# Kernel optimization log

Hardware: AMD Instinct MI355X
Metric: run time of the kernel (lower is better)

The kernel has to match this reference:

```python
import jax, jax.numpy as jnp
import numpy as np

B, T, C = 16, 2048, 384
E = 8          # num_experts
TOP_K = 2
CAP_F = 1.0
D_FF = 4 * C   # 1536


def setup_inputs() -> dict:
    key = jax.random.key(0)
    ks = jax.random.split(key, 10)
    s = 0.02
    return {
        "x": jax.random.normal(ks[0], (B, T, C), dtype=jnp.float32),
        "noise": jax.random.normal(ks[1], (B, T, E), dtype=jnp.float32),
        "w_route": jax.random.normal(ks[2], (C, E), dtype=jnp.float32) * s,
        "b_route": jnp.zeros((E,), dtype=jnp.float32),
        "w_noise": jax.random.normal(ks[3], (C, E), dtype=jnp.float32) * s,
        "b_noise": jnp.zeros((E,), dtype=jnp.float32),
        "w1": jax.random.normal(ks[4], (E, C, D_FF), dtype=jnp.float32) * s,
        "b1": jnp.zeros((E, D_FF), dtype=jnp.float32),
        "w2": jax.random.normal(ks[5], (E, D_FF, C), dtype=jnp.float32) * s,
        "b2": jnp.zeros((E, C), dtype=jnp.float32),
    }


def _moe_forward(x, noise, w_route, b_route, w_noise, b_noise, w1, b1, w2, b2):
    Bx, Tx, Cx = x.shape
    N = Bx * Tx
    cap = int(N * TOP_K / E * CAP_F)  # static expert capacity

    # --- NoisyTopkRouter ---
    logits = jnp.einsum('btc,ce->bte', x, w_route) + b_route
    noise_logits = jnp.einsum('btc,ce->bte', x, w_noise) + b_noise
    noisy = logits + noise * jax.nn.softplus(noise_logits)
    topv, topi = jax.lax.top_k(noisy, TOP_K)                    # [B,T,K]
    keep_mask = jnp.any(jax.nn.one_hot(topi, E, dtype=jnp.bool_), axis=-2)  # [B,T,E]
    sparse_logits = jnp.where(keep_mask, noisy, -jnp.inf)
    gating = jax.nn.softmax(sparse_logits, axis=-1)             # [B,T,E]

    # --- dispatch by top-1 expert with capacity drop (eval: dropout off) ---
    flat_x = x.reshape(N, Cx)
    flat_g = gating.reshape(N, E)
    top1 = jnp.argmax(flat_g, axis=-1)                          # [N]
    token_ids = jnp.arange(N, dtype=jnp.int32)
    out = jnp.zeros_like(flat_x)

    for i in range(E):
        mask = top1 == i                                        # [N]
        pos = jnp.cumsum(mask) - 1                              # rank within expert
        keep = mask & (pos < cap)
        slot = jnp.where(keep, pos, cap)                        # overflow -> dummy slot
        buf = jnp.zeros((cap + 1,), dtype=jnp.int32).at[slot].set(token_ids)
        idx = buf[:cap]                                         # token id per capacity slot
        valid = (jnp.arange(cap) < jnp.sum(keep))[:, None]      # [cap,1]
        xi = flat_x[idx]                                        # [cap,C] gather
        h = jnp.square(jax.nn.relu(xi @ w1[i] + b1[i]))         # ReLU^2
        yi = h @ w2[i] + b2[i]                                  # [cap,C]
        weighted = yi * flat_g[idx, i][:, None] * valid
        out = out.at[idx].add(weighted)                         # scatter-add

    return out.reshape(Bx, Tx, Cx)


def reference(x, noise, w_route, b_route, w_noise, b_noise, w1, b1, w2, b2):
    return _moe_forward(x, noise, w_route, b_route, w_noise, b_noise, w1, b1, w2, b2)
```

## Files before the change

kernel.cpp:

```cpp
#include <hip/hip_runtime.h>
#include <stdint.h>

#define E_NUM 8
#define CAP 8192
#define NTOK 32768
#define CDIM 384
#define DFF 1536
#define CNT_PAD 64

typedef unsigned short u16;
typedef __attribute__((ext_vector_type(8))) short short8;
typedef __attribute__((ext_vector_type(4))) float f32x4;

__device__ inline u16 f2bf(float f) {
    uint32_t u = __builtin_bit_cast(uint32_t, f);
    u += 0x7fffu + ((u >> 16) & 1u);
    return (u16)(u >> 16);
}

__device__ inline void gload_lds16(const void* g, void* l) {
    __builtin_amdgcn_global_load_lds(
        (const __attribute__((address_space(1))) void*)(uintptr_t)g,
        (__attribute__((address_space(3))) void*)(uint32_t)(uintptr_t)l,
        16, 0, 0);
}

__device__ inline void expert_span(const int* __restrict__ cnt, int e,
                                   int& base, int& n_e) {
    base = 0; n_e = 0;
#pragma unroll
    for (int i = 0; i < E_NUM; ++i) {
        int n = min(cnt[i * CNT_PAD], CAP);
        if (i < e) base += (n + 127) & ~127;
        else if (i == e) n_e = n;
    }
}

#define RT_TOK 64
#define RT_KC 64
#define RT_XS 68

__global__ __launch_bounds__(256, 3) void routing_kernel(
    const float* __restrict__ x, const float* __restrict__ noise,
    const float* __restrict__ w_route, const float* __restrict__ b_route,
    const float* __restrict__ w_noise, const float* __restrict__ b_noise,
    int* __restrict__ cnt, int* __restrict__ list, float* __restrict__ gate,
    u16* __restrict__ xbf)
{
    __shared__ float xs[RT_TOK * RT_XS];
    __shared__ float ws_r[CDIM * E_NUM];
    __shared__ float ws_n[CDIM * E_NUM];
    int tid = threadIdx.x;
    int lane = tid & 63;
    int seg = __builtin_amdgcn_readfirstlane(tid >> 6);
    int tok = tid & 63;
    int t0 = blockIdx.x * RT_TOK;

#pragma unroll
    for (int i = 0; i < 3; ++i) {
        int idx = tid + i * 256;
        *(float4*)&ws_r[idx * 4] = ((const float4*)w_route)[idx];
        *(float4*)&ws_n[idx * 4] = ((const float4*)w_noise)[idx];
    }

    int srow = tid >> 4;
    int scol = (tid & 15) * 4;

    float ar[E_NUM], an[E_NUM];
#pragma unroll
    for (int e = 0; e < E_NUM; ++e) { ar[e] = 0.f; an[e] = 0.f; }

    for (int c = 0; c < CDIM / RT_KC; ++c) {
        __syncthreads();
#pragma unroll
        for (int p = 0; p < 4; ++p) {
            int row = p * 16 + srow;
            float4 v = *(const float4*)(x + (size_t)(t0 + row) * CDIM + c * RT_KC + scol);
            *(float4*)&xs[row * RT_XS + scol] = v;
            uint2 b;
            b.x = (uint32_t)f2bf(v.x) | ((uint32_t)f2bf(v.y) << 16);
            b.y = (uint32_t)f2bf(v.z) | ((uint32_t)f2bf(v.w) << 16);
            *(uint2*)(xbf + (size_t)(t0 + row) * CDIM + c * RT_KC + scol) = b;
        }
        __syncthreads();
#pragma unroll
        for (int q = 0; q < 4; ++q) {
            float4 xq = *(const float4*)&xs[tok * RT_XS + seg * 16 + q * 4];
            int kb = c * RT_KC + seg * 16 + q * 4;
#pragma unroll
            for (int jj = 0; jj < 4; ++jj) {
                const float* wrk = &ws_r[(kb + jj) * E_NUM];
                const float* wnk = &ws_n[(kb + jj) * E_NUM];
                float4 wa = *(const float4*)wrk, wb = *(const float4*)(wrk + 4);
                float4 na = *(const float4*)wnk, nb = *(const float4*)(wnk + 4);
                float xk = (jj == 0) ? xq.x : (jj == 1) ? xq.y : (jj == 2) ? xq.z : xq.w;
                ar[0] += xk * wa.x; ar[1] += xk * wa.y; ar[2] += xk * wa.z; ar[3] += xk * wa.w;
                ar[4] += xk * wb.x; ar[5] += xk * wb.y; ar[6] += xk * wb.z; ar[7] += xk * wb.w;
                an[0] += xk * na.x; an[1] += xk * na.y; an[2] += xk * na.z; an[3] += xk * na.w;
                an[4] += xk * nb.x; an[5] += xk * nb.y; an[6] += xk * nb.z; an[7] += xk * nb.w;
            }
        }
    }
    __syncthreads();
    float* part = xs;
    float* pp = part + (size_t)(seg * 64 + tok) * 16;
    *(f32x4*)&pp[0]  = (f32x4){ar[0], ar[1], ar[2], ar[3]};
    *(f32x4*)&pp[4]  = (f32x4){ar[4], ar[5], ar[6], ar[7]};
    *(f32x4*)&pp[8]  = (f32x4){an[0], an[1], an[2], an[3]};
    *(f32x4*)&pp[12] = (f32x4){an[4], an[5], an[6], an[7]};
    __syncthreads();
    if (seg == 0) {
        int t = t0 + lane;
        float sr[E_NUM], sn[E_NUM];
#pragma unroll
        for (int e = 0; e < E_NUM; ++e) { sr[e] = b_route[e]; sn[e] = b_noise[e]; }
#pragma unroll
        for (int s = 0; s < 4; ++s) {
            const float* q = part + (size_t)(s * 64 + lane) * 16;
#pragma unroll
            for (int e = 0; e < E_NUM; ++e) { sr[e] += q[e]; sn[e] += q[8 + e]; }
        }
        float nz[E_NUM];
        const float* np = noise + (size_t)t * E_NUM;
#pragma unroll
        for (int e = 0; e < E_NUM; ++e) {
            float s = sn[e];
            float sp = fmaxf(s, 0.f) + __logf(1.f + __expf(-fabsf(s)));
            nz[e] = sr[e] + np[e] * sp;
        }
        float v1 = -1e30f; int i1 = 0;
#pragma unroll
        for (int e = 0; e < E_NUM; ++e) if (nz[e] > v1) { v1 = nz[e]; i1 = e; }
        float v2 = -1e30f;
#pragma unroll
        for (int e = 0; e < E_NUM; ++e) if (e != i1 && nz[e] > v2) v2 = nz[e];
        gate[t] = 1.f / (1.f + __expf(v2 - v1));
#pragma unroll
        for (int e = 0; e < E_NUM; ++e) {
            unsigned long long m = __ballot(i1 == e);
            if (m == 0) continue;
            int cnum = __popcll(m);
            int leader = __ffsll((long long)m) - 1;
            int basec = 0;
            if (lane == leader) basec = atomicAdd(&cnt[e * CNT_PAD], cnum);
            basec = __shfl(basec, leader);
            if (i1 == e) {
                int pos = basec + __popcll(m & ((1ull << lane) - 1ull));
                if (pos < CAP) list[e * CAP + pos] = t;
            }
        }
    }
}

__global__ __launch_bounds__(256) void transpose_cvt_kernel(
    const float* __restrict__ w1, u16* __restrict__ W1t,
    const float* __restrict__ w2, u16* __restrict__ W2t)
{
    __shared__ float tile[32][33];
    int z = blockIdx.z;
    const float* in; u16* out; int R, S, r0, c0;
    if (z < E_NUM) {
        in = w1 + (size_t)z * CDIM * DFF;  out = W1t + (size_t)z * CDIM * DFF;
        R = CDIM; S = DFF;
        c0 = blockIdx.x * 32; r0 = blockIdx.y * 32;
    } else {
        in = w2 + (size_t)(z - E_NUM) * DFF * CDIM;
        out = W2t + (size_t)(z - E_NUM) * DFF * CDIM;
        R = DFF; S = CDIM;
        r0 = blockIdx.x * 32; c0 = blockIdx.y * 32;
    }
    int tx = threadIdx.x, ty = threadIdx.y;
#pragma unroll
    for (int i = ty; i < 32; i += 8)
        tile[i][tx] = in[(size_t)(r0 + i) * S + (c0 + tx)];
    __syncthreads();
#pragma unroll
    for (int i = ty; i < 32; i += 8)
        out[(size_t)(c0 + i) * R + (r0 + tx)] = f2bf(tile[tx][i]);
}

template <int KD, int ND, bool FFN1>
__global__ __launch_bounds__(256, 2) void gemm_kernel(
    const u16* __restrict__ A, const u16* __restrict__ Bt,
    const float* __restrict__ bias, u16* __restrict__ H, float* __restrict__ Out,
    const int* __restrict__ cnt, const int* __restrict__ list,
    const float* __restrict__ gate)
{
    constexpr int NT = ND / 128;
    int bid = blockIdx.x;
    int xcd = bid & 7, slot = bid >> 3;
    int n_idx = slot % NT;
    int mglob = xcd + 8 * (slot / NT);
    int e = mglob >> 6;
    int m0 = (mglob & 63) * 128;
    int base, n_e;
    expert_span(cnt, e, base, n_e);
    int pad_e = (n_e + 127) & ~127;
    if (m0 >= pad_e) return;
    const u16* Be = Bt + ((size_t)e * ND + (size_t)n_idx * 128) * KD;

    __shared__ __align__(16) u16 As[2][128 * 64];
    __shared__ __align__(16) u16 Bs[2][128 * 64];
    __shared__ int s_tok[128];

    int tid = threadIdx.x;
    int w = tid >> 6, lane = tid & 63;
    int quad = lane >> 4, l15 = lane & 15;
    int wr = w & 1, wc = w >> 1;

    int srow = tid >> 3;
    int gcol = ((tid & 7) ^ ((tid >> 3) & 7)) * 8;

    if (FFN1) {
        if (tid < 128) {
            int rr = m0 + tid;
            s_tok[tid] = (rr < n_e) ? list[(size_t)e * CAP + rr] : NTOK;
        }
        __syncthreads();
    }
    const u16* Arow[4];
#pragma unroll
    for (int i = 0; i < 4; ++i) {
        int row = i * 32 + srow;
        if (FFN1) Arow[i] = A + (size_t)s_tok[row] * KD;
        else      Arow[i] = A + (size_t)(base + m0 + row) * KD;
    }

    auto stage = [&](int buf, int kb) {
#pragma unroll
        for (int i = 0; i < 4; ++i) {
            gload_lds16(Arow[i] + kb * 64 + gcol, &As[buf][i * 2048 + tid * 8]);
            gload_lds16(Be + (size_t)(i * 32 + srow) * KD + kb * 64 + gcol,
                        &Bs[buf][i * 2048 + tid * 8]);
        }
    };

    f32x4 acc[4][4];
    f32x4 zero = {0.f, 0.f, 0.f, 0.f};
#pragma unroll
    for (int a = 0; a < 4; ++a)
#pragma unroll
        for (int b = 0; b < 4; ++b) acc[a][b] = zero;

    constexpr int NK = KD / 64;
    stage(0, 0);
#pragma unroll 2
    for (int kb = 0; kb < NK; ++kb) {
        const int cur = kb & 1;
        if (kb + 1 < NK) {
            stage(cur ^ 1, kb + 1);
            asm volatile("s_waitcnt vmcnt(8)" ::: "memory");
        } else {
            asm volatile("s_waitcnt vmcnt(0)" ::: "memory");
        }
        __builtin_amdgcn_s_barrier();
        __builtin_amdgcn_sched_barrier(0);
#pragma unroll
        for (int h = 0; h < 2; ++h) {
            int pga = (((h * 4 + quad) ^ (l15 & 7))) * 8;
            short8 af[4], bf[4];
#pragma unroll
            for (int t = 0; t < 4; ++t) {
                af[t] = *(const short8*)&As[cur][(wr * 64 + t * 16 + l15) * 64 + pga];
                bf[t] = *(const short8*)&Bs[cur][(wc * 64 + t * 16 + l15) * 64 + pga];
            }
#pragma unroll
            for (int mt = 0; mt < 4; ++mt)
#pragma unroll
                for (int nt = 0; nt < 4; ++nt)
                    acc[mt][nt] = __builtin_amdgcn_mfma_f32_16x16x32_bf16(
                        af[mt], bf[nt], acc[mt][nt], 0, 0, 0);
        }
        __builtin_amdgcn_sched_barrier(0);
        __builtin_amdgcn_s_barrier();
        __builtin_amdgcn_sched_barrier(0);
    }

    int n0 = n_idx * 128;
    if (FFN1) {
        u16* Hs = (u16*)&As[0][0];
#pragma unroll
        for (int mt = 0; mt < 4; ++mt) {
            int rowL = wr * 64 + mt * 16 + quad * 4;
#pragma unroll
            for (int nt = 0; nt < 4; ++nt) {
                int colL = wc * 64 + nt * 16 + l15;
                float b = bias[(size_t)e * ND + n0 + colL];
#pragma unroll
                for (int r = 0; r < 4; ++r) {
                    float v = acc[mt][nt][r] + b;
                    v = fmaxf(v, 0.f);
                    int row = rowL + r;
                    Hs[row * 128 + (colL ^ ((row & 7) << 3))] = f2bf(v * v);
                }
            }
        }
        __syncthreads();
        u16* He = H + (size_t)(base + m0) * ND + n0;
#pragma unroll
        for (int j = 0; j < 8; ++j) {
            int idx = tid + j * 256;
            int row = idx >> 4;
            int c8 = (idx & 15) * 8;
            *(f32x4*)(He + (size_t)row * ND + c8) =
                *(const f32x4*)(Hs + row * 128 + (c8 ^ ((row & 7) << 3)));
        }
    } else {
#pragma unroll
        for (int mt = 0; mt < 4; ++mt) {
            int rowL = wr * 64 + mt * 16 + quad * 4;
#pragma unroll
            for (int r = 0; r < 4; ++r) {
                int rr = m0 + rowL + r;
                if (rr < n_e) {
                    int tok = list[(size_t)e * CAP + rr];
                    float g = gate[tok];
#pragma unroll
                    for (int nt = 0; nt < 4; ++nt) {
                        int col = n0 + wc * 64 + nt * 16 + l15;
                        float v = acc[mt][nt][r] + bias[(size_t)e * ND + col];
                        Out[(size_t)tok * CDIM + col] = v * g;
                    }
                }
            }
        }
    }
}

extern "C" void kernel_launch(void* const* d_in, const int* in_sizes, int n_in,
                              void* d_out, int out_size, void* d_ws, size_t ws_size,
                              hipStream_t stream)
{
    const float* x       = (const float*)d_in[0];
    const float* noise   = (const float*)d_in[1];
    const float* w_route = (const float*)d_in[2];
    const float* b_route = (const float*)d_in[3];
    const float* w_noise = (const float*)d_in[4];
    const float* b_noise = (const float*)d_in[5];
    const float* w1      = (const float*)d_in[6];
    const float* b1      = (const float*)d_in[7];
    const float* w2      = (const float*)d_in[8];
    const float* b2      = (const float*)d_in[9];
    float* out = (float*)d_out;

    char* ws = (char*)d_ws;
    size_t off = 0;
    auto alloc = [&](size_t bytes) {
        char* p = ws + off;
        off += (bytes + 255) & ~(size_t)255;
        return p;
    };
    int*   cnt  = (int*)alloc((size_t)E_NUM * CNT_PAD * sizeof(int));
    int*   list = (int*)alloc((size_t)E_NUM * CAP * sizeof(int));
    float* gate = (float*)alloc((size_t)NTOK * sizeof(float));
    u16*   W1t  = (u16*)alloc((size_t)E_NUM * DFF * CDIM * 2);
    u16*   W2t  = (u16*)alloc((size_t)E_NUM * CDIM * DFF * 2);

    u16* Xbf = (u16*)alloc((size_t)(NTOK + 1) * CDIM * 2);
    size_t rows = NTOK + E_NUM * 128;
    u16* Hb = (u16*)alloc(rows * DFF * 2);

    hipMemsetAsync(cnt, 0, (size_t)E_NUM * CNT_PAD * sizeof(int), stream);
    hipMemsetAsync(Xbf + (size_t)NTOK * CDIM, 0, CDIM * 2, stream);

    routing_kernel<<<NTOK / RT_TOK, 256, 0, stream>>>(x, noise, w_route, b_route,
                                                      w_noise, b_noise, cnt, list, gate, Xbf);
    transpose_cvt_kernel<<<dim3(48, 12, 16), dim3(32, 8), 0, stream>>>(w1, W1t, w2, W2t);

    gemm_kernel<CDIM, DFF, true><<<dim3((DFF / 128) * 512), 256, 0, stream>>>(
        Xbf, W1t, b1, Hb, nullptr, cnt, list, nullptr);
    gemm_kernel<DFF, CDIM, false><<<dim3((CDIM / 128) * 512), 256, 0, stream>>>(
        Hb, W2t, b2, nullptr, out, cnt, list, gate);
}
```

Baseline: 301.9 us.

## Fuse weight transpose into routing kernel and use 512-thread GEMM blocks

Merges the weight transpose/bf16 conversion into the routing kernel as extra blocks, which removes one kernel launch and lets both kinds of work run together. The GEMMs now use 512 threads (8 waves) per 128x128 tile, so each wave computes a 64x32 sub-tile and issues fewer loads. The aim is more waves in flight to hide latency. Padding rows now read from a dedicated zeroed dummy row, and the two memsets become one. The trade-off is a smaller per-wave tile with less register reuse and the same LDS footprint per block, which may cap occupancy.

```diff
diff --git a/kernel.cpp b/kernel.cpp
--- a/kernel.cpp
+++ b/kernel.cpp
@@ -39,22 +39,57 @@
 #define RT_TOK 64
 #define RT_KC 64
 #define RT_XS 68
-
-__global__ __launch_bounds__(256, 3) void routing_kernel(
+#define RT_BLOCKS (NTOK / RT_TOK)
+#define TR_BLOCKS (48 * 12 * 16)
+
+__global__ __launch_bounds__(256, 3) void route_prep_kernel(
     const float* __restrict__ x, const float* __restrict__ noise,
     const float* __restrict__ w_route, const float* __restrict__ b_route,
     const float* __restrict__ w_noise, const float* __restrict__ b_noise,
     int* __restrict__ cnt, int* __restrict__ list, float* __restrict__ gate,
-    u16* __restrict__ xbf)
+    u16* __restrict__ xbf,
+    const float* __restrict__ w1, u16* __restrict__ W1t,
+    const float* __restrict__ w2, u16* __restrict__ W2t)
 {
     __shared__ float xs[RT_TOK * RT_XS];
     __shared__ float ws_r[CDIM * E_NUM];
     __shared__ float ws_n[CDIM * E_NUM];
+    __shared__ float tile[32][33];
     int tid = threadIdx.x;
+    int bid = blockIdx.x;
+
+    if (bid >= RT_BLOCKS) {
+        int b = bid - RT_BLOCKS;
+        int z = b / 576;
+        int rem = b % 576;
+        int by = rem / 48, bx = rem % 48;
+        const float* in; u16* out; int S, r0, c0;
+        if (z < E_NUM) {
+            in = w1 + (size_t)z * CDIM * DFF;  out = W1t + (size_t)z * CDIM * DFF;
+            S = DFF;
+            c0 = bx * 32; r0 = by * 32;
+        } else {
+            in = w2 + (size_t)(z - E_NUM) * DFF * CDIM;
+            out = W2t + (size_t)(z - E_NUM) * DFF * CDIM;
+            S = CDIM;
+            r0 = bx * 32; c0 = by * 32;
+        }
+        int R = (z < E_NUM) ? CDIM : DFF;
+        int tx = tid & 31, ty = tid >> 5;
+#pragma unroll
+        for (int i = ty; i < 32; i += 8)
+            tile[i][tx] = in[(size_t)(r0 + i) * S + (c0 + tx)];
+        __syncthreads();
+#pragma unroll
+        for (int i = ty; i < 32; i += 8)
+            out[(size_t)(c0 + i) * R + (r0 + tx)] = f2bf(tile[tx][i]);
+        return;
+    }
+
     int lane = tid & 63;
     int seg = __builtin_amdgcn_readfirstlane(tid >> 6);
     int tok = tid & 63;
-    int t0 = blockIdx.x * RT_TOK;
+    int t0 = bid * RT_TOK;
 
 #pragma unroll
     for (int i = 0; i < 3; ++i) {
@@ -152,39 +187,12 @@
     }
 }
 
-__global__ __launch_bounds__(256) void transpose_cvt_kernel(
-    const float* __restrict__ w1, u16* __restrict__ W1t,
-    const float* __restrict__ w2, u16* __restrict__ W2t)
-{
-    __shared__ float tile[32][33];
-    int z = blockIdx.z;
-    const float* in; u16* out; int R, S, r0, c0;
-    if (z < E_NUM) {
-        in = w1 + (size_t)z * CDIM * DFF;  out = W1t + (size_t)z * CDIM * DFF;
-        R = CDIM; S = DFF;
-        c0 = blockIdx.x * 32; r0 = blockIdx.y * 32;
-    } else {
-        in = w2 + (size_t)(z - E_NUM) * DFF * CDIM;
-        out = W2t + (size_t)(z - E_NUM) * DFF * CDIM;
-        R = DFF; S = CDIM;
-        r0 = blockIdx.x * 32; c0 = blockIdx.y * 32;
-    }
-    int tx = threadIdx.x, ty = threadIdx.y;
-#pragma unroll
-    for (int i = ty; i < 32; i += 8)
-        tile[i][tx] = in[(size_t)(r0 + i) * S + (c0 + tx)];
-    __syncthreads();
-#pragma unroll
-    for (int i = ty; i < 32; i += 8)
-        out[(size_t)(c0 + i) * R + (r0 + tx)] = f2bf(tile[tx][i]);
-}
-
 template <int KD, int ND, bool FFN1>
-__global__ __launch_bounds__(256, 2) void gemm_kernel(
+__global__ __launch_bounds__(512, 4) void gemm_kernel(
     const u16* __restrict__ A, const u16* __restrict__ Bt,
     const float* __restrict__ bias, u16* __restrict__ H, float* __restrict__ Out,
     const int* __restrict__ cnt, const int* __restrict__ list,
-    const float* __restrict__ gate)
+    const float* __restrict__ gate, const u16* __restrict__ dummy)
 {
     constexpr int NT = ND / 128;
     int bid = blockIdx.x;
@@ -206,41 +214,46 @@
     int tid = threadIdx.x;
     int w = tid >> 6, lane = tid & 63;
     int quad = lane >> 4, l15 = lane & 15;
-    int wr = w & 1, wc = w >> 1;
+    int wr = w & 1;
+    int wc = w >> 1;
 
     int srow = tid >> 3;
-    int gcol = ((tid & 7) ^ ((tid >> 3) & 7)) * 8;
+    int gcol = ((tid & 7) ^ (srow & 7)) * 8;
 
     if (FFN1) {
         if (tid < 128) {
             int rr = m0 + tid;
-            s_tok[tid] = (rr < n_e) ? list[(size_t)e * CAP + rr] : NTOK;
-        }
-        __syncthreads();
-    }
-    const u16* Arow[4];
-#pragma unroll
-    for (int i = 0; i < 4; ++i) {
-        int row = i * 32 + srow;
-        if (FFN1) Arow[i] = A + (size_t)s_tok[row] * KD;
-        else      Arow[i] = A + (size_t)(base + m0 + row) * KD;
+            s_tok[tid] = (rr < n_e) ? list[(size_t)e * CAP + rr] : -1;
+        }
+        __syncthreads();
+    }
+    const u16* Arow[2];
+#pragma unroll
+    for (int i = 0; i < 2; ++i) {
+        int row = i * 64 + srow;
+        if (FFN1) {
+            int s = s_tok[row];
+            Arow[i] = (s >= 0) ? A + (size_t)s * KD : dummy;
+        } else {
+            Arow[i] = A + (size_t)(base + m0 + row) * KD;
+        }
     }
 
     auto stage = [&](int buf, int kb) {
 #pragma unroll
-        for (int i = 0; i < 4; ++i) {
-            gload_lds16(Arow[i] + kb * 64 + gcol, &As[buf][i * 2048 + tid * 8]);
-            gload_lds16(Be + (size_t)(i * 32 + srow) * KD + kb * 64 + gcol,
-                        &Bs[buf][i * 2048 + tid * 8]);
+        for (int i = 0; i < 2; ++i) {
+            gload_lds16(Arow[i] + kb * 64 + gcol, &As[buf][i * 4096 + tid * 8]);
+            gload_lds16(Be + (size_t)(i * 64 + srow) * KD + kb * 64 + gcol,
+                        &Bs[buf][i * 4096 + tid * 8]);
         }
     };
 
-    f32x4 acc[4][4];
+    f32x4 acc[4][2];
     f32x4 zero = {0.f, 0.f, 0.f, 0.f};
 #pragma unroll
     for (int a = 0; a < 4; ++a)
 #pragma unroll
-        for (int b = 0; b < 4; ++b) acc[a][b] = zero;
+        for (int b = 0; b < 2; ++b) acc[a][b] = zero;
 
     constexpr int NK = KD / 64;
     stage(0, 0);
@@ -249,7 +262,7 @@
         const int cur = kb & 1;
         if (kb + 1 < NK) {
             stage(cur ^ 1, kb + 1);
-            asm volatile("s_waitcnt vmcnt(8)" ::: "memory");
+            asm volatile("s_waitcnt vmcnt(4)" ::: "memory");
         } else {
             asm volatile("s_waitcnt vmcnt(0)" ::: "memory");
         }
@@ -257,17 +270,18 @@
         __builtin_amdgcn_sched_barrier(0);
 #pragma unroll
         for (int h = 0; h < 2; ++h) {
-            int pga = (((h * 4 + quad) ^ (l15 & 7))) * 8;
-            short8 af[4], bf[4];
-#pragma unroll
-            for (int t = 0; t < 4; ++t) {
+            int pga = ((h * 4 + quad) ^ (l15 & 7)) * 8;
+            short8 af[4], bf[2];
+#pragma unroll
+            for (int t = 0; t < 4; ++t)
                 af[t] = *(const short8*)&As[cur][(wr * 64 + t * 16 + l15) * 64 + pga];
-                bf[t] = *(const short8*)&Bs[cur][(wc * 64 + t * 16 + l15) * 64 + pga];
-            }
+#pragma unroll
+            for (int t = 0; t < 2; ++t)
+                bf[t] = *(const short8*)&Bs[cur][(wc * 32 + t * 16 + l15) * 64 + pga];
 #pragma unroll
             for (int mt = 0; mt < 4; ++mt)
 #pragma unroll
-                for (int nt = 0; nt < 4; ++nt)
+                for (int nt = 0; nt < 2; ++nt)
                     acc[mt][nt] = __builtin_amdgcn_mfma_f32_16x16x32_bf16(
                         af[mt], bf[nt], acc[mt][nt], 0, 0, 0);
         }
@@ -283,8 +297,8 @@
         for (int mt = 0; mt < 4; ++mt) {
             int rowL = wr * 64 + mt * 16 + quad * 4;
 #pragma unroll
-            for (int nt = 0; nt < 4; ++nt) {
-                int colL = wc * 64 + nt * 16 + l15;
+            for (int nt = 0; nt < 2; ++nt) {
+                int colL = wc * 32 + nt * 16 + l15;
                 float b = bias[(size_t)e * ND + n0 + colL];
 #pragma unroll
                 for (int r = 0; r < 4; ++r) {
@@ -298,8 +312,8 @@
         __syncthreads();
         u16* He = H + (size_t)(base + m0) * ND + n0;
 #pragma unroll
-        for (int j = 0; j < 8; ++j) {
-            int idx = tid + j * 256;
+        for (int j = 0; j < 4; ++j) {
+            int idx = tid + j * 512;
             int row = idx >> 4;
             int c8 = (idx & 15) * 8;
             *(f32x4*)(He + (size_t)row * ND + c8) =
@@ -316,8 +330,8 @@
                     int tok = list[(size_t)e * CAP + rr];
                     float g = gate[tok];
 #pragma unroll
-                    for (int nt = 0; nt < 4; ++nt) {
-                        int col = n0 + wc * 64 + nt * 16 + l15;
+                    for (int nt = 0; nt < 2; ++nt) {
+                        int col = n0 + wc * 32 + nt * 16 + l15;
                         float v = acc[mt][nt][r] + bias[(size_t)e * ND + col];
                         Out[(size_t)tok * CDIM + col] = v * g;
                     }
@@ -350,25 +364,24 @@
         off += (bytes + 255) & ~(size_t)255;
         return p;
     };
-    int*   cnt  = (int*)alloc((size_t)E_NUM * CNT_PAD * sizeof(int));
-    int*   list = (int*)alloc((size_t)E_NUM * CAP * sizeof(int));
-    float* gate = (float*)alloc((size_t)NTOK * sizeof(float));
-    u16*   W1t  = (u16*)alloc((size_t)E_NUM * DFF * CDIM * 2);
-    u16*   W2t  = (u16*)alloc((size_t)E_NUM * CDIM * DFF * 2);
-
-    u16* Xbf = (u16*)alloc((size_t)(NTOK + 1) * CDIM * 2);
+    int*   cnt   = (int*)alloc((size_t)E_NUM * CNT_PAD * sizeof(int));
+    u16*   dummy = (u16*)alloc((size_t)CDIM * 2);
+    int*   list  = (int*)alloc((size_t)E_NUM * CAP * sizeof(int));
+    float* gate  = (float*)alloc((size_t)NTOK * sizeof(float));
+    u16*   W1t   = (u16*)alloc((size_t)E_NUM * DFF * CDIM * 2);
+    u16*   W2t   = (u16*)alloc((size_t)E_NUM * CDIM * DFF * 2);
+    u16*   Xbf   = (u16*)alloc((size_t)NTOK * CDIM * 2);
     size_t rows = NTOK + E_NUM * 128;
-    u16* Hb = (u16*)alloc(rows * DFF * 2);
-
-    hipMemsetAsync(cnt, 0, (size_t)E_NUM * CNT_PAD * sizeof(int), stream);
-    hipMemsetAsync(Xbf + (size_t)NTOK * CDIM, 0, CDIM * 2, stream);
-
-    routing_kernel<<<NTOK / RT_TOK, 256, 0, stream>>>(x, noise, w_route, b_route,
-                                                      w_noise, b_noise, cnt, list, gate, Xbf);
-    transpose_cvt_kernel<<<dim3(48, 12, 16), dim3(32, 8), 0, stream>>>(w1, W1t, w2, W2t);
-
-    gemm_kernel<CDIM, DFF, true><<<dim3((DFF / 128) * 512), 256, 0, stream>>>(
-        Xbf, W1t, b1, Hb, nullptr, cnt, list, nullptr);
-    gemm_kernel<DFF, CDIM, false><<<dim3((CDIM / 128) * 512), 256, 0, stream>>>(
-        Hb, W2t, b2, nullptr, out, cnt, list, gate);
-}
+    u16*   Hb    = (u16*)alloc(rows * DFF * 2);
+
+    hipMemsetAsync(ws, 0, (size_t)E_NUM * CNT_PAD * sizeof(int) + CDIM * 2, stream);
+
+    route_prep_kernel<<<RT_BLOCKS + TR_BLOCKS, 256, 0, stream>>>(
+        x, noise, w_route, b_route, w_noise, b_noise, cnt, list, gate, Xbf,
+        w1, W1t, w2, W2t);
+
+    gemm_kernel<CDIM, DFF, true><<<dim3((DFF / 128) * 512), 512, 0, stream>>>(
+        Xbf, W1t, b1, Hb, nullptr, cnt, list, nullptr, dummy);
+    gemm_kernel<DFF, CDIM, false><<<dim3((CDIM / 128) * 512), 512, 0, stream>>>(
+        Hb, W2t, b2, nullptr, out, cnt, list, gate, nullptr);
+}
```

Result: no change. 301.5 us (-0.1%).
